# Kernel tuning notes

Measured on AMD Instinct MI355X. Metric: run time of the kernel, lower is better.

The kernel has to match this reference:

```python
import jax, jax.numpy as jnp
import numpy as np

N = 50000      # num nodes
E = 800000     # num edges (before self loops)
DIN = 128      # input_dim
HID = 32       # hidden_dim per head
HEADS = 4
DOUT = 128     # output_dim
NEG_SLOPE = 0.2
EPS = 1e-5


def setup_inputs() -> dict:
    key = jax.random.key(0)
    ks = jax.random.split(key, 16)
    s = 0.05
    return {
        "x": jax.random.normal(ks[0], (N, DIN), dtype=jnp.float32),
        "edge_index": jax.random.randint(ks[1], (2, E), 0, N, dtype=jnp.int64),
        # GAT layer 1 (heads=4, concat=True)
        "W1": jax.random.normal(ks[2], (DIN, HEADS * HID), dtype=jnp.float32) * s,
        "att_src1": jax.random.normal(ks[3], (HEADS, HID), dtype=jnp.float32) * s,
        "att_dst1": jax.random.normal(ks[4], (HEADS, HID), dtype=jnp.float32) * s,
        "b1": jnp.zeros((HEADS * HID,), dtype=jnp.float32),
        # GAT layer 2 (heads=1, concat=False)
        "W2": jax.random.normal(ks[5], (HEADS * HID, DOUT), dtype=jnp.float32) * s,
        "att_src2": jax.random.normal(ks[6], (1, DOUT), dtype=jnp.float32) * s,
        "att_dst2": jax.random.normal(ks[7], (1, DOUT), dtype=jnp.float32) * s,
        "b2": jnp.zeros((DOUT,), dtype=jnp.float32),
        # LayerNorms
        "g1": jnp.ones((HEADS * HID,), dtype=jnp.float32),
        "be1": jnp.zeros((HEADS * HID,), dtype=jnp.float32),
        "g2": jnp.ones((DOUT,), dtype=jnp.float32),
        "be2": jnp.zeros((DOUT,), dtype=jnp.float32),
    }


def gat_conv(x, src, dst, W, a_src, a_dst, n_nodes):
    # x: [N, Fin]; W: [Fin, H*C]; a_src/a_dst: [H, C]
    H, C = a_src.shape
    h = (x @ W).reshape(-1, H, C)                       # [N, H, C]
    es = jnp.einsum("nhc,hc->nh", h, a_src)             # [N, H]
    ed = jnp.einsum("nhc,hc->nh", h, a_dst)             # [N, H]
    e = jax.nn.leaky_relu(es[src] + ed[dst], NEG_SLOPE)  # [E, H]
    # segment softmax over incoming edges of each dst node
    m = jax.ops.segment_max(e, dst, num_segments=n_nodes)
    a = jnp.exp(e - jax.lax.stop_gradient(m)[dst])
    den = jax.ops.segment_sum(a, dst, num_segments=n_nodes)
    alpha = a / den[dst]                                 # [E, H]
    out = jax.ops.segment_sum(alpha[:, :, None] * h[src], dst,
                              num_segments=n_nodes)      # [N, H, C]
    return out


def layer_norm(x, g, b):
    mu = jnp.mean(x, axis=-1, keepdims=True)
    var = jnp.mean((x - mu) ** 2, axis=-1, keepdims=True)
    return (x - mu) * jax.lax.rsqrt(var + EPS) * g + b


def reference(x, edge_index, W1, att_src1, att_dst1, b1,
              W2, att_src2, att_dst2, b2, g1, be1, g2, be2):
    n = x.shape[0]
    loop = jnp.arange(n, dtype=edge_index.dtype)
    src = jnp.concatenate([edge_index[0], loop])  # PyG add_self_loops=True
    dst = jnp.concatenate([edge_index[1], loop])

    h = gat_conv(x, src, dst, W1, att_src1, att_dst1, n)   # [N, 4, 32]
    h = h.reshape(n, -1) + b1                              # concat=True
    h = jax.nn.relu(layer_norm(h, g1, be1))                # dropout = id (eval)

    o = gat_conv(h, src, dst, W2, att_src2, att_dst2, n)   # [N, 1, DOUT]
    o = o[:, 0, :] + b2                                    # concat=False, 1 head
    o = jax.nn.relu(layer_norm(o, g2, be2))
    return o
```

## Files before the change

kernel.cpp:

```cpp
#include <hip/hip_runtime.h>

#define NEG 0.2f
#define LNEPS 1e-5f
#define BCAP 5120

static __device__ __forceinline__ float leaky(float e){ return fmaxf(e, NEG*e); }

static __device__ __forceinline__ unsigned pack_bf16(float a, float b){
  unsigned ua = __float_as_uint(a), ub = __float_as_uint(b);
  ua += 0x7FFFu + ((ua>>16)&1u);
  ub += 0x7FFFu + ((ub>>16)&1u);
  return (ua>>16) | (ub & 0xFFFF0000u);
}
static __device__ __forceinline__ float lo_bf(unsigned u){ return __uint_as_float(u<<16); }
static __device__ __forceinline__ float hi_bf(unsigned u){ return __uint_as_float(u & 0xFFFF0000u); }

typedef float f32x4 __attribute__((ext_vector_type(4)));
typedef short s16x8 __attribute__((ext_vector_type(8)));
union U4V8 { uint4 u; s16x8 v; };

static __device__ __forceinline__ void acc8(float w, uint4 u, float* a){
  a[0] = fmaf(w, lo_bf(u.x), a[0]);
  a[1] = fmaf(w, hi_bf(u.x), a[1]);
  a[2] = fmaf(w, lo_bf(u.y), a[2]);
  a[3] = fmaf(w, hi_bf(u.y), a[3]);
  a[4] = fmaf(w, lo_bf(u.z), a[4]);
  a[5] = fmaf(w, hi_bf(u.z), a[5]);
  a[6] = fmaf(w, lo_bf(u.w), a[6]);
  a[7] = fmaf(w, hi_bf(u.w), a[7]);
}

static __device__ __forceinline__ void wave_scan256(int* sm, int t){
  if (t < 64){
    int a0=sm[t*4], a1=sm[t*4+1], a2=sm[t*4+2], a3=sm[t*4+3];
    int s = a0+a1+a2+a3, sc = s;
    #pragma unroll
    for (int o=1;o<64;o<<=1){ int x = __shfl_up(sc, o); if (t >= o) sc += x; }
    int e = sc - s;
    sm[t*4]   = e;
    sm[t*4+1] = e + a0;
    sm[t*4+2] = e + a0 + a1;
    sm[t*4+3] = e + a0 + a1 + a2;
  }
}


static __device__ __forceinline__ void wprep_body(int i, const float* __restrict__ W1,
                                                  const float* __restrict__ W2,
                                                  uint4* __restrict__ W1b, uint4* __restrict__ W2b){
  const float* W = (i < 2048) ? W1 : W2;
  uint4* Wb = (i < 2048) ? W1b : W2b;
  int ii = i & 2047;
  int lane = ii & 63, t = (ii>>6)&7, k0 = ii>>9;
  int c = lane & 15, q = lane >> 4;
  const float* base = &W[(size_t)(k0*32 + q*8)*128 + t*16 + c];
  uint4 u;
  u.x = pack_bf16(base[0*128], base[1*128]);
  u.y = pack_bf16(base[2*128], base[3*128]);
  u.z = pack_bf16(base[4*128], base[5*128]);
  u.w = pack_bf16(base[6*128], base[7*128]);
  Wb[ii] = u;
}

static __device__ void bstage_body(int bb, const int* __restrict__ src, const int* __restrict__ dst,
                                   int* __restrict__ bfill, unsigned* __restrict__ stage, int E){
  __shared__ int h[256];
  __shared__ int sm[256];
  __shared__ int sb[256];
  __shared__ int cur[256];
  __shared__ int rb[256];
  __shared__ unsigned buf[2048];
  int t = threadIdx.x;
  h[t] = 0; __syncthreads();
  int base = bb * 2048;
  int cnt = min(2048, E - base);
  for (int i = t; i < cnt; i += 256) atomicAdd(&h[((unsigned)dst[base+i]) >> 8], 1);
  __syncthreads();
  int hv = h[t];
  sm[t] = hv; __syncthreads();
  wave_scan256(sm, t);
  __syncthreads();
  int excl = sm[t];
  sb[t] = excl;
  cur[t] = excl;
  rb[t] = (hv > 0) ? atomicAdd(&bfill[t], hv) : 0;
  __syncthreads();
  for (int i = t; i < cnt; i += 256){
    unsigned d = (unsigned)dst[base+i];
    unsigned v = (unsigned)src[base+i] | (d << 16);
    int p = atomicAdd(&cur[d >> 8], 1);
    buf[p] = v;
  }
  __syncthreads();
  for (int i = t; i < cnt; i += 256){
    unsigned v = buf[i];
    int b = v >> 24;
    int slot = rb[b] + (i - sb[b]);
    if (slot < BCAP) stage[(size_t)b*BCAP + slot] = v;
  }
}

static __device__ void bucket_body(int b, const unsigned* __restrict__ stage, const int* __restrict__ bfill,
                                   int* __restrict__ offA, int* __restrict__ offB,
                                   unsigned* __restrict__ csr2, int N){
  __shared__ int cnt[256];
  __shared__ int sm[256];
  __shared__ int cur[256];
  int t = threadIdx.x;
  int lo = b * BCAP;
  int hi = lo + min(bfill[b], BCAP);
  cnt[t] = 0; __syncthreads();
  for (int i = lo + t; i < hi; i += 256) atomicAdd(&cnt[(stage[i] >> 16) & 0xFF], 1);
  __syncthreads();
  sm[t] = cnt[t]; __syncthreads();
  wave_scan256(sm, t);
  __syncthreads();
  int ex = sm[t];
  cur[t] = ex;
  int d = (b << 8) + t;
  if (d < N){ offA[d] = lo + ex; offB[d] = lo + ex + cnt[t]; }
  __syncthreads();
  for (int i = lo + t; i < hi; i += 256){
    unsigned v = stage[i];
    int p = atomicAdd(&cur[(v >> 16) & 0xFF], 1);
    csr2[(size_t)(lo + p)] = v;
  }
}

template<int HEADS, bool PACKED>
static __device__ void gemm_body(int bid, const float* __restrict__ A, const unsigned* __restrict__ Ab,
                                 const uint4* __restrict__ Wb,
                                 const float* __restrict__ as, const float* __restrict__ ad,
                                 unsigned* __restrict__ Hb, float* __restrict__ es,
                                 float* __restrict__ ed, float* __restrict__ m0, int n){
  __shared__ unsigned hstage[4][16*68];
  int tid = threadIdx.x;
  int wave = tid >> 6, lane = tid & 63;
  int c = lane & 15, q = lane >> 4;
  int r0 = bid*64 + wave*16;
  int rowa = r0 + c;
  int rowc = min(rowa, n-1);
  f32x4 acc[8];
  #pragma unroll
  for (int t=0;t<8;++t) acc[t] = (f32x4){0.f,0.f,0.f,0.f};

  #pragma unroll
  for (int k0 = 0; k0 < 4; ++k0){
    U4V8 af;
    if (PACKED){
      af.u = *(const uint4*)&Ab[(size_t)rowc*64 + k0*16 + q*4];
    } else {
      const float* ap = &A[(size_t)rowc*128 + k0*32 + q*8];
      float4 v0 = *(const float4*)ap;
      float4 v1 = *(const float4*)(ap+4);
      af.u.x = pack_bf16(v0.x, v0.y);
      af.u.y = pack_bf16(v0.z, v0.w);
      af.u.z = pack_bf16(v1.x, v1.y);
      af.u.w = pack_bf16(v1.z, v1.w);
    }
    #pragma unroll
    for (int t=0;t<8;++t){
      U4V8 bf;
      bf.u = Wb[(k0*8+t)*64 + lane];
      acc[t] = __builtin_amdgcn_mfma_f32_16x16x32_bf16(af.v, bf.v, acc[t], 0, 0, 0);
    }
  }

  float asv[8], adv[8];
  #pragma unroll
  for (int t=0;t<8;++t){ asv[t] = as[t*16+c]; adv[t] = ad[t*16+c]; }
  if (HEADS == 4){
    float pes[4][4], ped[4][4];
    #pragma unroll
    for (int r=0;r<4;++r)
      #pragma unroll
      for (int h=0;h<4;++h){ pes[r][h]=0.f; ped[r][h]=0.f; }
    #pragma unroll
    for (int t=0;t<8;++t)
      #pragma unroll
      for (int r=0;r<4;++r){
        pes[r][t>>1] = fmaf(acc[t][r], asv[t], pes[r][t>>1]);
        ped[r][t>>1] = fmaf(acc[t][r], adv[t], ped[r][t>>1]);
      }
    #pragma unroll
    for (int r=0;r<4;++r)
      #pragma unroll
      for (int h=0;h<4;++h){
        #pragma unroll
        for (int m=1;m<16;m<<=1){
          pes[r][h] += __shfl_xor(pes[r][h], m);
          ped[r][h] += __shfl_xor(ped[r][h], m);
        }
      }
    if (c == 0){
      #pragma unroll
      for (int r=0;r<4;++r){
        int row2 = r0 + q*4 + r;
        if (row2 < n){
          float4 e = make_float4(pes[r][0],pes[r][1],pes[r][2],pes[r][3]);
          float4 d = make_float4(ped[r][0],ped[r][1],ped[r][2],ped[r][3]);
          float4 mm = make_float4(leaky(e.x+d.x),leaky(e.y+d.y),leaky(e.z+d.z),leaky(e.w+d.w));
          *(float4*)&es[(size_t)row2*4] = e;
          *(float4*)&ed[(size_t)row2*4] = d;
          *(float4*)&m0[(size_t)row2*4] = mm;
        }
      }
    }
  } else {
    float pes[4] = {0.f,0.f,0.f,0.f}, ped[4] = {0.f,0.f,0.f,0.f};
    #pragma unroll
    for (int t=0;t<8;++t)
      #pragma unroll
      for (int r=0;r<4;++r){
        pes[r] = fmaf(acc[t][r], asv[t], pes[r]);
        ped[r] = fmaf(acc[t][r], adv[t], ped[r]);
      }
    #pragma unroll
    for (int r=0;r<4;++r){
      #pragma unroll
      for (int m=1;m<16;m<<=1){
        pes[r] += __shfl_xor(pes[r], m);
        ped[r] += __shfl_xor(ped[r], m);
      }
    }
    if (c == 0){
      #pragma unroll
      for (int r=0;r<4;++r){
        int row2 = r0 + q*4 + r;
        if (row2 < n){
          es[row2] = pes[r]; ed[row2] = ped[r]; m0[row2] = leaky(pes[r]+ped[r]);
        }
      }
    }
  }

  unsigned* hs = hstage[wave];
  #pragma unroll
  for (int t=0;t<8;++t)
    #pragma unroll
    for (int r=0;r<4;++r){
      float other = __shfl_xor(acc[t][r], 1);
      if (!(c & 1)) hs[(q*4+r)*68 + t*8 + (c>>1)] = pack_bf16(acc[t][r], other);
    }
  #pragma unroll
  for (int it=0; it<4; ++it){
    int idx = it*64 + lane;
    int rr = idx >> 4, c4 = idx & 15;
    int grow = r0 + rr;
    if (grow < n)
      *(uint4*)&Hb[(size_t)grow*64 + c4*4] = *(uint4*)&hs[rr*68 + c4*4];
  }
}


__global__ __launch_bounds__(256) void k_A(const float* __restrict__ W1, const float* __restrict__ W2,
                                           uint4* __restrict__ W1b, uint4* __restrict__ W2b,
                                           const int* __restrict__ src, const int* __restrict__ dst,
                                           int* __restrict__ bfill, unsigned* __restrict__ stage, int E){
  int bid = blockIdx.x;
  if (bid < 16){
    wprep_body(bid*256 + threadIdx.x, W1, W2, W1b, W2b);
  } else {
    bstage_body(bid - 16, src, dst, bfill, stage, E);
  }
}

__global__ __launch_bounds__(256) void k_B(const float* __restrict__ x, const uint4* __restrict__ W1b,
                                           const float* __restrict__ as1, const float* __restrict__ ad1,
                                           unsigned* __restrict__ Hb, float* __restrict__ es1,
                                           float* __restrict__ ed1, float* __restrict__ m01,
                                           const unsigned* __restrict__ stage, const int* __restrict__ bfill,
                                           int* __restrict__ offA, int* __restrict__ offB,
                                           unsigned* __restrict__ csr2, int N, int gb){
  int bid = blockIdx.x;
  if (bid < gb){
    gemm_body<4,false>(bid, x, nullptr, W1b, as1, ad1, Hb, es1, ed1, m01, N);
  } else {
    bucket_body(bid - gb, stage, bfill, offA, offB, csr2, N);
  }
}

template<int HEADS, bool PACKED>
__global__ __launch_bounds__(256) void k_gemm_mfma(const float* __restrict__ A,
                                                   const unsigned* __restrict__ Ab,
                                                   const uint4* __restrict__ Wb,
                                                   const float* __restrict__ as, const float* __restrict__ ad,
                                                   unsigned* __restrict__ Hb, float* __restrict__ es,
                                                   float* __restrict__ ed, float* __restrict__ m0, int n){
  gemm_body<HEADS,PACKED>(blockIdx.x, A, Ab, Wb, as, ad, Hb, es, ed, m0, n);
}


template<bool OUT_PACKED>
__global__ __launch_bounds__(256) void k_agg4(const unsigned* __restrict__ Hb,
                                              const float* __restrict__ es, const float* __restrict__ ed,
                                              const float* __restrict__ m0,
                                              const int* __restrict__ offA, const int* __restrict__ offB,
                                              const unsigned* __restrict__ csr2,
                                              const float* __restrict__ bias, const float* __restrict__ g,
                                              const float* __restrict__ be, float* __restrict__ out,
                                              unsigned* __restrict__ outp, int N){
  int lane = threadIdx.x & 63;
  int node = blockIdx.x*4 + (threadIdx.x >> 6);
  if (node >= N) return;
  int grp = lane >> 4;
  int fi  = lane & 15;
  int hsrc = (fi >> 2) << 4;
  float edn = ed[(size_t)node*4 + grp];
  float m0n = m0[(size_t)node*4 + grp];
  float a[8];
  #pragma unroll
  for (int k=0;k<8;++k) a[k] = 0.f;
  float l = 0.f;
  int j0 = offA[node], j1 = offB[node];
  for (int c0 = j0; c0 < j1; c0 += 16){
    int m = j1 - c0;
    int sv = 0; float wv = 0.f;
    if (fi < m){
      unsigned v = csr2[c0 + fi];
      sv = v & 0xFFFF;
      wv = __expf(leaky(es[(size_t)sv*4 + grp] + edn) - m0n);
    }
    int   s0 = __shfl(sv, grp),          s1 = __shfl(sv, 4 + grp),
          s2 = __shfl(sv, 8 + grp),      s3 = __shfl(sv, 12 + grp);
    float w0 = __shfl(wv, hsrc + grp),   w1 = __shfl(wv, hsrc + 4 + grp),
          w2 = __shfl(wv, hsrc + 8 + grp), w3 = __shfl(wv, hsrc + 12 + grp);
    uint4 u0 = *(const uint4*)&Hb[(size_t)s0*64 + fi*4];
    uint4 u1 = *(const uint4*)&Hb[(size_t)s1*64 + fi*4];
    uint4 u2 = *(const uint4*)&Hb[(size_t)s2*64 + fi*4];
    uint4 u3 = *(const uint4*)&Hb[(size_t)s3*64 + fi*4];
    l += ((w0 + w1) + (w2 + w3));
    acc8(w0, u0, a);
    acc8(w1, u1, a);
    acc8(w2, u2, a);
    acc8(w3, u3, a);
  }
  #pragma unroll
  for (int k=0;k<8;++k){
    a[k] += __shfl_xor(a[k], 16);
    a[k] += __shfl_xor(a[k], 32);
  }
  l += __shfl_xor(l, 16);
  l += __shfl_xor(l, 32);
  uint4 us = *(const uint4*)&Hb[(size_t)node*64 + fi*4];
  a[0] += lo_bf(us.x); a[1] += hi_bf(us.x);
  a[2] += lo_bf(us.y); a[3] += hi_bf(us.y);
  a[4] += lo_bf(us.z); a[5] += hi_bf(us.z);
  a[6] += lo_bf(us.w); a[7] += hi_bf(us.w);
  l += 1.f;

  float rl = __frcp_rn(l);
  float4 bv0 = *(const float4*)&bias[fi*8];
  float4 bv1 = *(const float4*)&bias[fi*8 + 4];
  float v[8];
  v[0] = a[0]*rl + bv0.x; v[1] = a[1]*rl + bv0.y;
  v[2] = a[2]*rl + bv0.z; v[3] = a[3]*rl + bv0.w;
  v[4] = a[4]*rl + bv1.x; v[5] = a[5]*rl + bv1.y;
  v[6] = a[6]*rl + bv1.z; v[7] = a[7]*rl + bv1.w;
  float s = ((v[0]+v[1])+(v[2]+v[3])) + ((v[4]+v[5])+(v[6]+v[7]));
  #pragma unroll
  for (int mm=1; mm<16; mm<<=1) s += __shfl_xor(s, mm);
  float mu = s * (1.f/128.f);
  float d[8], ss = 0.f;
  #pragma unroll
  for (int k=0;k<8;++k){ d[k] = v[k]-mu; ss += d[k]*d[k]; }
  #pragma unroll
  for (int mm=1; mm<16; mm<<=1) ss += __shfl_xor(ss, mm);
  float rs = rsqrtf(ss*(1.f/128.f) + LNEPS);
  float4 gv0 = *(const float4*)&g[fi*8];
  float4 gv1 = *(const float4*)&g[fi*8 + 4];
  float4 ev0 = *(const float4*)&be[fi*8];
  float4 ev1 = *(const float4*)&be[fi*8 + 4];
  float y[8];
  y[0] = fmaxf(d[0]*rs*gv0.x + ev0.x, 0.f);
  y[1] = fmaxf(d[1]*rs*gv0.y + ev0.y, 0.f);
  y[2] = fmaxf(d[2]*rs*gv0.z + ev0.z, 0.f);
  y[3] = fmaxf(d[3]*rs*gv0.w + ev0.w, 0.f);
  y[4] = fmaxf(d[4]*rs*gv1.x + ev1.x, 0.f);
  y[5] = fmaxf(d[5]*rs*gv1.y + ev1.y, 0.f);
  y[6] = fmaxf(d[6]*rs*gv1.z + ev1.z, 0.f);
  y[7] = fmaxf(d[7]*rs*gv1.w + ev1.w, 0.f);
  if (grp == 0){
    if (OUT_PACKED){
      uint4 o;
      o.x = pack_bf16(y[0], y[1]);
      o.y = pack_bf16(y[2], y[3]);
      o.z = pack_bf16(y[4], y[5]);
      o.w = pack_bf16(y[6], y[7]);
      *(uint4*)&outp[(size_t)node*64 + fi*4] = o;
    } else {
      *(float4*)&out[(size_t)node*128 + fi*8]     = make_float4(y[0],y[1],y[2],y[3]);
      *(float4*)&out[(size_t)node*128 + fi*8 + 4] = make_float4(y[4],y[5],y[6],y[7]);
    }
  }
}

__global__ __launch_bounds__(256) void k_agg1(const unsigned* __restrict__ Hb,
                                              const float* __restrict__ es, const float* __restrict__ ed,
                                              const float* __restrict__ m0,
                                              const int* __restrict__ offA, const int* __restrict__ offB,
                                              const unsigned* __restrict__ csr2,
                                              const float* __restrict__ bias, const float* __restrict__ g,
                                              const float* __restrict__ be, float* __restrict__ out, int N){
  int lane = threadIdx.x & 63;
  int node = blockIdx.x*4 + (threadIdx.x >> 6);
  if (node >= N) return;
  int grp = lane >> 4;
  int fi  = lane & 15;
  float edn = ed[node];
  float m0n = m0[node];
  float a[8];
  #pragma unroll
  for (int k=0;k<8;++k) a[k] = 0.f;
  float l = 0.f;
  int j0 = offA[node], j1 = offB[node];
  for (int c0 = j0; c0 < j1; c0 += 64){
    int m = min(64, j1 - c0);
    int sv = 0; float wv = 0.f;
    if (lane < m){
      unsigned v = csr2[c0 + lane];
      sv = v & 0xFFFF;
      wv = __expf(leaky(es[sv] + edn) - m0n);
    }
    for (int jj = 0; jj < m; jj += 16){
      int   s0 = __shfl(sv, jj + grp),      s1 = __shfl(sv, jj + 4 + grp),
            s2 = __shfl(sv, jj + 8 + grp),  s3 = __shfl(sv, jj + 12 + grp);
      float w0 = __shfl(wv, jj + grp),      w1 = __shfl(wv, jj + 4 + grp),
            w2 = __shfl(wv, jj + 8 + grp),  w3 = __shfl(wv, jj + 12 + grp);
      uint4 u0 = *(const uint4*)&Hb[(size_t)s0*64 + fi*4];
      uint4 u1 = *(const uint4*)&Hb[(size_t)s1*64 + fi*4];
      uint4 u2 = *(const uint4*)&Hb[(size_t)s2*64 + fi*4];
      uint4 u3 = *(const uint4*)&Hb[(size_t)s3*64 + fi*4];
      l += ((w0 + w1) + (w2 + w3));
      acc8(w0, u0, a);
      acc8(w1, u1, a);
      acc8(w2, u2, a);
      acc8(w3, u3, a);
    }
  }
  #pragma unroll
  for (int k=0;k<8;++k){
    a[k] += __shfl_xor(a[k], 16);
    a[k] += __shfl_xor(a[k], 32);
  }
  l += __shfl_xor(l, 16);
  l += __shfl_xor(l, 32);
  uint4 us = *(const uint4*)&Hb[(size_t)node*64 + fi*4];
  a[0] += lo_bf(us.x); a[1] += hi_bf(us.x);
  a[2] += lo_bf(us.y); a[3] += hi_bf(us.y);
  a[4] += lo_bf(us.z); a[5] += hi_bf(us.z);
  a[6] += lo_bf(us.w); a[7] += hi_bf(us.w);
  l += 1.f;

  float rl = __frcp_rn(l);
  float4 bv0 = *(const float4*)&bias[fi*8];
  float4 bv1 = *(const float4*)&bias[fi*8 + 4];
  float v2[8];
  v2[0] = a[0]*rl + bv0.x; v2[1] = a[1]*rl + bv0.y;
  v2[2] = a[2]*rl + bv0.z; v2[3] = a[3]*rl + bv0.w;
  v2[4] = a[4]*rl + bv1.x; v2[5] = a[5]*rl + bv1.y;
  v2[6] = a[6]*rl + bv1.z; v2[7] = a[7]*rl + bv1.w;
  float s = ((v2[0]+v2[1])+(v2[2]+v2[3])) + ((v2[4]+v2[5])+(v2[6]+v2[7]));
  #pragma unroll
  for (int mm=1; mm<16; mm<<=1) s += __shfl_xor(s, mm);
  float mu = s * (1.f/128.f);
  float d[8], ss = 0.f;
  #pragma unroll
  for (int k=0;k<8;++k){ d[k] = v2[k]-mu; ss += d[k]*d[k]; }
  #pragma unroll
  for (int mm=1; mm<16; mm<<=1) ss += __shfl_xor(ss, mm);
  float rs = rsqrtf(ss*(1.f/128.f) + LNEPS);
  float4 gv0 = *(const float4*)&g[fi*8];
  float4 gv1 = *(const float4*)&g[fi*8 + 4];
  float4 ev0 = *(const float4*)&be[fi*8];
  float4 ev1 = *(const float4*)&be[fi*8 + 4];
  float y[8];
  y[0] = fmaxf(d[0]*rs*gv0.x + ev0.x, 0.f);
  y[1] = fmaxf(d[1]*rs*gv0.y + ev0.y, 0.f);
  y[2] = fmaxf(d[2]*rs*gv0.z + ev0.z, 0.f);
  y[3] = fmaxf(d[3]*rs*gv0.w + ev0.w, 0.f);
  y[4] = fmaxf(d[4]*rs*gv1.x + ev1.x, 0.f);
  y[5] = fmaxf(d[5]*rs*gv1.y + ev1.y, 0.f);
  y[6] = fmaxf(d[6]*rs*gv1.z + ev1.z, 0.f);
  y[7] = fmaxf(d[7]*rs*gv1.w + ev1.w, 0.f);
  if (grp == 0){
    *(float4*)&out[(size_t)node*128 + fi*8]     = make_float4(y[0],y[1],y[2],y[3]);
    *(float4*)&out[(size_t)node*128 + fi*8 + 4] = make_float4(y[4],y[5],y[6],y[7]);
  }
}


extern "C" void kernel_launch(void* const* d_in, const int* in_sizes, int n_in,
                              void* d_out, int out_size, void* d_ws, size_t ws_size,
                              hipStream_t stream){
  const float* x   = (const float*)d_in[0];
  const int*   ei  = (const int*)  d_in[1];
  const float* W1  = (const float*)d_in[2];
  const float* as1 = (const float*)d_in[3];
  const float* ad1 = (const float*)d_in[4];
  const float* b1  = (const float*)d_in[5];
  const float* W2  = (const float*)d_in[6];
  const float* as2 = (const float*)d_in[7];
  const float* ad2 = (const float*)d_in[8];
  const float* b2  = (const float*)d_in[9];
  const float* g1  = (const float*)d_in[10];
  const float* be1 = (const float*)d_in[11];
  const float* g2  = (const float*)d_in[12];
  const float* be2 = (const float*)d_in[13];

  int N = in_sizes[0] / 128;
  int E = in_sizes[1] / 2;
  const int* src = ei;
  const int* dst = ei + E;

  int NB = (N + 255) >> 8;

  char* p = (char*)d_ws;
  auto carve = [&](size_t bytes)->char*{ char* r = p; p += ((bytes + 255) / 256) * 256; return r; };
  unsigned* Hb = (unsigned*)carve((size_t)N*64*4);
  unsigned* Bb = (unsigned*)carve((size_t)N*64*4);
  float* es1 = (float*)carve((size_t)N*4*4);
  float* ed1 = (float*)carve((size_t)N*4*4);
  float* m01 = (float*)carve((size_t)N*4*4);
  float* es2 = (float*)carve((size_t)N*4);
  float* ed2 = (float*)carve((size_t)N*4);
  float* m02 = (float*)carve((size_t)N*4);
  int* offA  = (int*)carve((size_t)N*4);
  int* offB  = (int*)carve((size_t)N*4);
  unsigned* stg  = (unsigned*)carve((size_t)NB*BCAP*4);
  unsigned* csr2 = (unsigned*)carve((size_t)NB*BCAP*4);
  uint4* W1b = (uint4*)carve(2048*16);
  uint4* W2b = (uint4*)carve(2048*16);
  int* bfill = (int*)carve(256*4);

  hipMemsetAsync(bfill, 0, 1024, stream);

  int nbe = (E + 2047) / 2048;
  int gb  = (N + 63) / 64;
  int nb4 = (N + 3) / 4;

  k_A<<<16 + nbe, 256, 0, stream>>>(W1, W2, W1b, W2b, src, dst, bfill, stg, E);
  k_B<<<gb + NB, 256, 0, stream>>>(x, W1b, as1, ad1, Hb, es1, ed1, m01,
                                   stg, bfill, offA, offB, csr2, N, gb);
  k_agg4<true><<<nb4, 256, 0, stream>>>(Hb, es1, ed1, m01, offA, offB, csr2,
                                        b1, g1, be1, nullptr, Bb, N);
  k_agg4<true><<<nb4, 256, 0, stream>>>(Hb, es1, ed1, m01, offA, offB, csr2,
                                        b1, g1, be1, nullptr, Bb, N);
  k_gemm_mfma<1,true><<<gb, 256, 0, stream>>>(nullptr, Bb, W2b, as2, ad2, Hb, es2, ed2, m02, N);
  k_agg1<<<nb4, 256, 0, stream>>>(Hb, es2, ed2, m02, offA, offB, csr2,
                                  b2, g2, be2, (float*)d_out, N);
}
```

Baseline: 264.5 us.

## Split edge bucketing into histogram, scan, and deterministic scatter kernels

Replaces the single edge-staging kernel, which reserved slots per bucket with global atomics on bfill, with three passes. The first writes per-block bucket histograms, the second prefix-scans them per bucket, and the third scatters edges to deterministic offsets, which also removes the memset. It also deletes a duplicated launch of the layer-1 aggregation kernel that recomputed the same output. The cost is two extra kernel launches and another read of dst.

```diff
diff --git a/kernel.cpp b/kernel.cpp
--- a/kernel.cpp
+++ b/kernel.cpp
@@ -62,29 +62,58 @@
   Wb[ii] = u;
 }
 
-static __device__ void bstage_body(int bb, const int* __restrict__ src, const int* __restrict__ dst,
-                                   int* __restrict__ bfill, unsigned* __restrict__ stage, int E){
+static __device__ void hist_body(int bb, const int* __restrict__ dst,
+                                 int* __restrict__ histT, int E, int nbe){
   __shared__ int h[256];
+  int t = threadIdx.x;
+  h[t] = 0; __syncthreads();
+  int base = bb * 2048;
+  int cnt = min(2048, E - base);
+  for (int i = t; i < cnt; i += 256) atomicAdd(&h[((unsigned)dst[base+i]) >> 8], 1);
+  __syncthreads();
+  histT[(size_t)t*nbe + bb] = h[t];
+}
+
+__global__ __launch_bounds__(256) void k_A2(const int* __restrict__ histT,
+                                            int* __restrict__ baseT,
+                                            int* __restrict__ bfill, int nbe){
+  int bucket = blockIdx.x*4 + (threadIdx.x >> 6);
+  int lane = threadIdx.x & 63;
+  const int* row = &histT[(size_t)bucket*nbe];
+  int* brow = &baseT[(size_t)bucket*nbe];
+  int carry = 0;
+  for (int c0 = 0; c0 < nbe; c0 += 64){
+    int idx = c0 + lane;
+    int v = (idx < nbe) ? row[idx] : 0;
+    int sc = v;
+    #pragma unroll
+    for (int o=1;o<64;o<<=1){ int x = __shfl_up(sc, o); if (lane >= o) sc += x; }
+    if (idx < nbe) brow[idx] = sc - v + carry;
+    carry += __shfl(sc, 63);
+  }
+  if (lane == 0) bfill[bucket] = carry;
+}
+
+static __device__ void stage3_body(int bb, const int* __restrict__ src, const int* __restrict__ dst,
+                                   const int* __restrict__ histT, const int* __restrict__ baseT,
+                                   unsigned* __restrict__ stage, int E, int nbe){
   __shared__ int sm[256];
   __shared__ int sb[256];
   __shared__ int cur[256];
   __shared__ int rb[256];
   __shared__ unsigned buf[2048];
   int t = threadIdx.x;
-  h[t] = 0; __syncthreads();
-  int base = bb * 2048;
-  int cnt = min(2048, E - base);
-  for (int i = t; i < cnt; i += 256) atomicAdd(&h[((unsigned)dst[base+i]) >> 8], 1);
-  __syncthreads();
-  int hv = h[t];
+  int hv = histT[(size_t)t*nbe + bb];
+  rb[t] = baseT[(size_t)t*nbe + bb];
   sm[t] = hv; __syncthreads();
   wave_scan256(sm, t);
   __syncthreads();
   int excl = sm[t];
   sb[t] = excl;
   cur[t] = excl;
-  rb[t] = (hv > 0) ? atomicAdd(&bfill[t], hv) : 0;
-  __syncthreads();
+  __syncthreads();
+  int base = bb * 2048;
+  int cnt = min(2048, E - base);
   for (int i = t; i < cnt; i += 256){
     unsigned d = (unsigned)dst[base+i];
     unsigned v = (unsigned)src[base+i] | (d << 16);
@@ -253,16 +282,22 @@
 }
 
 
-__global__ __launch_bounds__(256) void k_A(const float* __restrict__ W1, const float* __restrict__ W2,
-                                           uint4* __restrict__ W1b, uint4* __restrict__ W2b,
-                                           const int* __restrict__ src, const int* __restrict__ dst,
-                                           int* __restrict__ bfill, unsigned* __restrict__ stage, int E){
+__global__ __launch_bounds__(256) void k_A1(const float* __restrict__ W1, const float* __restrict__ W2,
+                                            uint4* __restrict__ W1b, uint4* __restrict__ W2b,
+                                            const int* __restrict__ dst,
+                                            int* __restrict__ histT, int E, int nbe){
   int bid = blockIdx.x;
   if (bid < 16){
     wprep_body(bid*256 + threadIdx.x, W1, W2, W1b, W2b);
   } else {
-    bstage_body(bid - 16, src, dst, bfill, stage, E);
-  }
+    hist_body(bid - 16, dst, histT, E, nbe);
+  }
+}
+
+__global__ __launch_bounds__(256) void k_A3(const int* __restrict__ src, const int* __restrict__ dst,
+                                            const int* __restrict__ histT, const int* __restrict__ baseT,
+                                            unsigned* __restrict__ stage, int E, int nbe){
+  stage3_body(blockIdx.x, src, dst, histT, baseT, stage, E, nbe);
 }
 
 __global__ __launch_bounds__(256) void k_B(const float* __restrict__ x, const uint4* __restrict__ W1b,
@@ -514,6 +549,9 @@
   const int* dst = ei + E;
 
   int NB = (N + 255) >> 8;
+  int nbe = (E + 2047) / 2048;
+  int gb  = (N + 63) / 64;
+  int nb4 = (N + 3) / 4;
 
   char* p = (char*)d_ws;
   auto carve = [&](size_t bytes)->char*{ char* r = p; p += ((bytes + 255) / 256) * 256; return r; };
@@ -532,18 +570,14 @@
   uint4* W1b = (uint4*)carve(2048*16);
   uint4* W2b = (uint4*)carve(2048*16);
   int* bfill = (int*)carve(256*4);
-
-  hipMemsetAsync(bfill, 0, 1024, stream);
-
-  int nbe = (E + 2047) / 2048;
-  int gb  = (N + 63) / 64;
-  int nb4 = (N + 3) / 4;
-
-  k_A<<<16 + nbe, 256, 0, stream>>>(W1, W2, W1b, W2b, src, dst, bfill, stg, E);
+  int* histT = (int*)carve((size_t)256*nbe*4);
+  int* baseT = (int*)carve((size_t)256*nbe*4);
+
+  k_A1<<<16 + nbe, 256, 0, stream>>>(W1, W2, W1b, W2b, dst, histT, E, nbe);
+  k_A2<<<64, 256, 0, stream>>>(histT, baseT, bfill, nbe);
+  k_A3<<<nbe, 256, 0, stream>>>(src, dst, histT, baseT, stg, E, nbe);
   k_B<<<gb + NB, 256, 0, stream>>>(x, W1b, as1, ad1, Hb, es1, ed1, m01,
                                    stg, bfill, offA, offB, csr2, N, gb);
-  k_agg4<true><<<nb4, 256, 0, stream>>>(Hb, es1, ed1, m01, offA, offB, csr2,
-                                        b1, g1, be1, nullptr, Bb, N);
   k_agg4<true><<<nb4, 256, 0, stream>>>(Hb, es1, ed1, m01, offA, offB, csr2,
                                         b1, g1, be1, nullptr, Bb, N);
   k_gemm_mfma<1,true><<<gb, 256, 0, stream>>>(nullptr, Bb, W2b, as2, ad2, Hb, es2, ed2, m02, N);
```

New measurement: 226.9 us. 14.2% less time.
